# Performance work log

Measured on AMD Instinct MI355X. Metric: run time of the kernel, lower is better.

## Reference

```python
import jax, jax.numpy as jnp
import numpy as np

N, E, D_IN, D_H, N_CLASSES = 50000, 800000, 128, 128, 40
D_OUT = D_H // 2
LN_EPS = 1e-5


def _seg_mean(msgs, dst, n_nodes):
    # mean aggregation over incoming edges; isolated nodes get 0 (like PyG mean)
    s = jax.ops.segment_sum(msgs, dst, num_segments=n_nodes)
    cnt = jax.ops.segment_sum(jnp.ones((dst.shape[0], 1), msgs.dtype), dst, num_segments=n_nodes)
    return s / jnp.maximum(cnt, 1.0)


def _sage(x, src, dst, Wl, bl, Wr):
    # PyG SAGEConv(mean): lin_l(mean_j x_j) + lin_r(x_i); lin_l has bias, lin_r none
    agg = _seg_mean(x[src], dst, x.shape[0])  # [N, d_in]
    return agg @ Wl + bl + x @ Wr


def _layernorm(x, g, b):
    mu = jnp.mean(x, axis=-1, keepdims=True)
    var = jnp.mean(jnp.square(x - mu), axis=-1, keepdims=True)
    return (x - mu) * jax.lax.rsqrt(var + LN_EPS) * g + b


def setup_inputs() -> dict:
    key = jax.random.key(0)
    ks = jax.random.split(key, 20)
    sc = lambda d: 1.0 / np.sqrt(d)
    inp = {
        "x": jax.random.normal(ks[0], (N, D_IN), dtype=jnp.float32),
        "edge_index": jax.random.randint(ks[1], (2, E), 0, N, dtype=jnp.int32),
        # block1 (in==hidden -> proj is Identity)
        "Wl1": jax.random.normal(ks[2], (D_IN, D_H), jnp.float32) * sc(D_IN),
        "bl1": jnp.zeros((D_H,), jnp.float32),
        "Wr1": jax.random.normal(ks[3], (D_IN, D_H), jnp.float32) * sc(D_IN),
        "g1": jnp.ones((D_H,), jnp.float32),
        "b1": jnp.zeros((D_H,), jnp.float32),
        # block2
        "Wl2": jax.random.normal(ks[4], (D_H, D_H), jnp.float32) * sc(D_H),
        "bl2": jnp.zeros((D_H,), jnp.float32),
        "Wr2": jax.random.normal(ks[5], (D_H, D_H), jnp.float32) * sc(D_H),
        "g2": jnp.ones((D_H,), jnp.float32),
        "b2": jnp.zeros((D_H,), jnp.float32),
        # conv_out: hidden -> hidden//2
        "Wl3": jax.random.normal(ks[6], (D_H, D_OUT), jnp.float32) * sc(D_H),
        "bl3": jnp.zeros((D_OUT,), jnp.float32),
        "Wr3": jax.random.normal(ks[7], (D_H, D_OUT), jnp.float32) * sc(D_H),
        # classifier: LayerNorm(D_OUT) + Linear(D_OUT, n_classes)
        "gc": jnp.ones((D_OUT,), jnp.float32),
        "bc": jnp.zeros((D_OUT,), jnp.float32),
        "Wc": jax.random.normal(ks[8], (D_OUT, N_CLASSES), jnp.float32) * sc(D_OUT),
        "bcls": jnp.zeros((N_CLASSES,), jnp.float32),
    }
    return inp


def reference(x, edge_index, Wl1, bl1, Wr1, g1, b1, Wl2, bl2, Wr2, g2, b2,
              Wl3, bl3, Wr3, gc, bc, Wc, bcls):
    src, dst = edge_index[0], edge_index[1]
    # block1: SAGE -> LN -> GELU -> (dropout eval=identity) -> +x (proj=Identity)
    h = _sage(x, src, dst, Wl1, bl1, Wr1)
    x = jax.nn.gelu(_layernorm(h, g1, b1), approximate=False) + x
    # block2
    h = _sage(x, src, dst, Wl2, bl2, Wr2)
    x = jax.nn.gelu(_layernorm(h, g2, b2), approximate=False) + x
    # conv_out + GELU
    x = jax.nn.gelu(_sage(x, src, dst, Wl3, bl3, Wr3), approximate=False)
    # classifier: LN then Linear
    return _layernorm(x, gc, bc) @ Wc + bcls
```

## Files before the change

kernel.cpp:

```cpp
#include <hip/hip_runtime.h>
#include <math.h>


typedef __attribute__((ext_vector_type(8))) short bf16x8;
typedef __attribute__((ext_vector_type(4))) float f32x4;

#define NWG 256
#define NBK 196
#define CAP2 6144

__device__ inline float gelu_f(float x) {
    return 0.5f * x * (1.0f + erff(x * 0.70710678118654752440f));
}

__device__ inline ushort f2b(float f) {
    uint u = __float_as_uint(f);
    u += 0x7fffu + ((u >> 16) & 1u);
    return (ushort)(u >> 16);
}

__device__ inline float b2f(ushort h) { return __uint_as_float((uint)h << 16); }


__global__ __launch_bounds__(256) void k_hist(const int* __restrict__ dst, int e,
                                              int* __restrict__ cnts) {
    __shared__ int h[NBK];
    const int tid = threadIdx.x;
    const int wg = blockIdx.x;
    for (int i = tid; i < NBK; i += 256) h[i] = 0;
    __syncthreads();
    const int ch = (e + NWG - 1) / NWG;
    const int lo = wg * ch;
    const int hi = min(e, lo + ch);
    for (int i = lo + tid; i < hi; i += 256) atomicAdd(&h[dst[i] >> 8], 1);
    __syncthreads();
    for (int i = tid; i < NBK; i += 256) cnts[i * NWG + wg] = h[i];
}

__global__ __launch_bounds__(256) void k_scanP1(const int* __restrict__ in,
                                                int* __restrict__ out,
                                                int* __restrict__ part, int m) {
    __shared__ int sm[256];
    const int tid = threadIdx.x;
    const int base = blockIdx.x * 1024 + tid * 4;
    int4 v = make_int4(0, 0, 0, 0);
    if (base + 3 < m) {
        v = *(const int4*)(in + base);
    } else {
        if (base + 0 < m) v.x = in[base + 0];
        if (base + 1 < m) v.y = in[base + 1];
        if (base + 2 < m) v.z = in[base + 2];
        if (base + 3 < m) v.w = in[base + 3];
    }
    int s = v.x + v.y + v.z + v.w;
    sm[tid] = s;
    __syncthreads();
#pragma unroll
    for (int d = 1; d < 256; d <<= 1) {
        int add = (tid >= d) ? sm[tid - d] : 0;
        __syncthreads();
        sm[tid] += add;
        __syncthreads();
    }
    int ex = (tid ? sm[tid - 1] : 0);
    if (base + 0 < m) out[base + 0] = ex;
    ex += v.x;
    if (base + 1 < m) out[base + 1] = ex;
    ex += v.y;
    if (base + 2 < m) out[base + 2] = ex;
    ex += v.z;
    if (base + 3 < m) out[base + 3] = ex;
    if (tid == 255) part[blockIdx.x] = sm[255];
}

__global__ __launch_bounds__(256) void k_scanP2(int* __restrict__ out,
                                                const int* __restrict__ part, int m) {
    const int tid = threadIdx.x;
    const int bid = blockIdx.x;
    const int lane = tid & 63;
    int s = 0;
    for (int j = lane; j < bid; j += 64) s += part[j];
#pragma unroll
    for (int d = 32; d > 0; d >>= 1) s += __shfl_xor(s, d);
    const int i0 = bid * 1024 + tid * 4;
#pragma unroll
    for (int j = 0; j < 4; ++j) {
        int i = i0 + j;
        if (i < m) out[i] += s;
    }
}

__global__ __launch_bounds__(256) void k_scat(const int* __restrict__ src,
                                              const int* __restrict__ dst, int e,
                                              const int* __restrict__ bases,
                                              uint* __restrict__ pairs) {
    __shared__ int cur[NBK];
    const int tid = threadIdx.x;
    const int wg = blockIdx.x;
    for (int i = tid; i < NBK; i += 256) cur[i] = bases[i * NWG + wg];
    __syncthreads();
    const int ch = (e + NWG - 1) / NWG;
    const int lo = wg * ch;
    const int hi = min(e, lo + ch);
    for (int i = lo + tid; i < hi; i += 256) {
        int d = dst[i];
        int pos = atomicAdd(&cur[d >> 8], 1);
        pairs[pos] = (uint)src[i] | ((uint)(d & 255) << 16);
    }
}

__global__ __launch_bounds__(256) void k_sortC(const uint* __restrict__ pairs,
                                               const int* __restrict__ bases, int e,
                                               int* __restrict__ csr, int* __restrict__ off,
                                               int* __restrict__ cntout, int n) {
    __shared__ int hist[256];
    __shared__ int curl[256];
    __shared__ int sm[256];
    __shared__ int buf[CAP2];
    const int bk = blockIdx.x;
    const int tid = threadIdx.x;
    const int start = bases[bk * NWG];
    const int end = (bk == NBK - 1) ? e : bases[(bk + 1) * NWG];
    int m = end - start;
    if (m > CAP2) m = CAP2;

    hist[tid] = 0;
    __syncthreads();
    for (int i = tid; i < m; i += 256) atomicAdd(&hist[(pairs[start + i] >> 16) & 255], 1);
    __syncthreads();
    int v = hist[tid];
    sm[tid] = v;
    __syncthreads();
#pragma unroll
    for (int d = 1; d < 256; d <<= 1) {
        int add = (tid >= d) ? sm[tid - d] : 0;
        __syncthreads();
        sm[tid] += add;
        __syncthreads();
    }
    int excl = sm[tid] - v;
    int node = (bk << 8) + tid;
    if (node < n) {
        off[node] = start + excl;
        cntout[node] = v;
    }
    curl[tid] = excl;
    __syncthreads();
    for (int i = tid; i < m; i += 256) {
        uint w = pairs[start + i];
        int pos = atomicAdd(&curl[(w >> 16) & 255], 1);
        buf[pos] = (int)(w & 0xffffu);
    }
    __syncthreads();
    for (int i = tid; i < m; i += 256) csr[start + i] = buf[i];
}


__global__ void k_cast(const float* __restrict__ in, ushort* __restrict__ out, int nvec4) {
    int t = blockIdx.x * blockDim.x + threadIdx.x;
    int stride = gridDim.x * blockDim.x;
    for (int i = t; i < nvec4; i += stride) {
        float4 v = ((const float4*)in)[i];
        ushort4 o;
        o.x = f2b(v.x);
        o.y = f2b(v.y);
        o.z = f2b(v.z);
        o.w = f2b(v.w);
        ((ushort4*)out)[i] = o;
    }
}

__global__ void k_wprep(const float* __restrict__ Wl, const float* __restrict__ Wr,
                        int KH, int C, ushort* __restrict__ Wt) {
    int t = blockIdx.x * blockDim.x + threadIdx.x;
    int total = C * 2 * KH;
    if (t >= total) return;
    int c = t / (2 * KH), k = t % (2 * KH);
    float v = (k < KH) ? Wl[(size_t)k * C + c] : Wr[(size_t)(k - KH) * C + c];
    Wt[t] = f2b(v);
}

__global__ void k_wprepC(const float* __restrict__ Wc, ushort* __restrict__ Wct) {
    int t = blockIdx.x * blockDim.x + threadIdx.x;
    if (t >= 64 * 64) return;
    int c = t >> 6, k = t & 63;
    float v = (c < 40) ? Wc[k * 40 + c] : 0.f;
    Wct[t] = f2b(v);
}


__global__ void k_agg(const ushort* __restrict__ X, const int* __restrict__ off,
                      const int* __restrict__ cnt, const int* __restrict__ csr,
                      ushort* __restrict__ agg, int n) {
    const int wid = (blockIdx.x * blockDim.x + threadIdx.x) >> 6;
    const int lane = threadIdx.x & 63;
    const int nw = (gridDim.x * blockDim.x) >> 6;
    for (int i = wid; i < n; i += nw) {
        int s0 = off[i];
        int deg = cnt[i];
        int c = 0;
        if (lane < deg) c = csr[s0 + lane];
        float a0 = 0.f, a1 = 0.f;
        const int dcap = deg < 64 ? deg : 64;
        int t = 0;
        for (; t + 3 < dcap; t += 4) {
            int i0 = __shfl(c, t), i1 = __shfl(c, t + 1);
            int i2 = __shfl(c, t + 2), i3 = __shfl(c, t + 3);
            uint u0 = *((const uint*)(X + (size_t)i0 * 128) + lane);
            uint u1 = *((const uint*)(X + (size_t)i1 * 128) + lane);
            uint u2 = *((const uint*)(X + (size_t)i2 * 128) + lane);
            uint u3 = *((const uint*)(X + (size_t)i3 * 128) + lane);
            a0 += __uint_as_float(u0 << 16) + __uint_as_float(u1 << 16) +
                  __uint_as_float(u2 << 16) + __uint_as_float(u3 << 16);
            a1 += __uint_as_float(u0 & 0xffff0000u) + __uint_as_float(u1 & 0xffff0000u) +
                  __uint_as_float(u2 & 0xffff0000u) + __uint_as_float(u3 & 0xffff0000u);
        }
        for (; t < dcap; ++t) {
            uint u0 = *((const uint*)(X + (size_t)__shfl(c, t) * 128) + lane);
            a0 += __uint_as_float(u0 << 16);
            a1 += __uint_as_float(u0 & 0xffff0000u);
        }
        for (int tt = s0 + 64; tt < s0 + deg; ++tt) {
            uint u0 = *((const uint*)(X + (size_t)csr[tt] * 128) + lane);
            a0 += __uint_as_float(u0 << 16);
            a1 += __uint_as_float(u0 & 0xffff0000u);
        }
        float inv = 1.0f / (float)(deg > 1 ? deg : 1);
        uint pk = (uint)f2b(a0 * inv) | ((uint)f2b(a1 * inv) << 16);
        *((uint*)(agg + (size_t)i * 128) + lane) = pk;
    }
}


template <int DOUT, int EPI>
__global__ __launch_bounds__(256) void k_gemm(
    const ushort* __restrict__ Agg, const ushort* __restrict__ Xb,
    const ushort* __restrict__ Wt, const float* __restrict__ bias,
    const float* __restrict__ g, const float* __restrict__ b,
    ushort* __restrict__ OutB, int n) {
    constexpr int CT = DOUT / 64;
    const int tid = threadIdx.x;
    const int wave = tid >> 6;
    const int lane = tid & 63;
    const int l16 = lane & 15;
    const int g4 = lane >> 4;
    const int row0 = blockIdx.x * 32;

    __shared__ __align__(16) ushort As[32 * 256];

    int colv[CT];
#pragma unroll
    for (int ct = 0; ct < CT; ++ct) colv[ct] = (wave * CT + ct) * 16 + l16;

    bf16x8 bfr[CT][8];
#pragma unroll
    for (int ct = 0; ct < CT; ++ct) {
        const ushort* wp = Wt + (size_t)colv[ct] * 256 + g4 * 8;
#pragma unroll
        for (int ks = 0; ks < 8; ++ks) bfr[ct][ks] = *(const bf16x8*)(wp + ks * 32);
    }

    {
        const int row = tid >> 3;
        const int jj = tid & 7;
        int gr = row0 + row;
        if (gr > n - 1) gr = n - 1;
        const ushort* pa = Agg + (size_t)gr * 128;
        const ushort* pb = Xb + (size_t)gr * 128;
        uint4 v0 = *(const uint4*)(pa + jj * 8);
        uint4 v1 = *(const uint4*)(pa + (jj + 8) * 8);
        uint4 v2 = *(const uint4*)(pb + jj * 8);
        uint4 v3 = *(const uint4*)(pb + (jj + 8) * 8);
        const int sw = (row & 7) << 4;
        char* lb = (char*)As + row * 512;
        *(uint4*)(lb + ((jj * 16) ^ sw)) = v0;
        *(uint4*)(lb + (((jj + 8) * 16) ^ sw)) = v1;
        *(uint4*)(lb + (((jj + 16) * 16) ^ sw)) = v2;
        *(uint4*)(lb + (((jj + 24) * 16) ^ sw)) = v3;
    }

    float biasv[CT], gv[CT], bbv[CT];
#pragma unroll
    for (int ct = 0; ct < CT; ++ct) {
        biasv[ct] = bias[colv[ct]];
        gv[ct] = g[colv[ct]];
        bbv[ct] = b[colv[ct]];
    }

    __syncthreads();

    f32x4 acc[2][CT];
#pragma unroll
    for (int rt = 0; rt < 2; ++rt)
#pragma unroll
        for (int ct = 0; ct < CT; ++ct) {
            acc[rt][ct][0] = 0.f;
            acc[rt][ct][1] = 0.f;
            acc[rt][ct][2] = 0.f;
            acc[rt][ct][3] = 0.f;
        }
#pragma unroll
    for (int ks = 0; ks < 8; ++ks) {
        bf16x8 a[2];
#pragma unroll
        for (int rt = 0; rt < 2; ++rt) {
            const int row = rt * 16 + l16;
            a[rt] = *(const bf16x8*)((const char*)As + row * 512 +
                                     ((ks * 64 + g4 * 16) ^ ((row & 7) << 4)));
        }
#pragma unroll
        for (int rt = 0; rt < 2; ++rt)
#pragma unroll
            for (int ct = 0; ct < CT; ++ct)
                acc[rt][ct] = __builtin_amdgcn_mfma_f32_16x16x32_bf16(a[rt], bfr[ct][ks],
                                                                     acc[rt][ct], 0, 0, 0);
    }

    __shared__ float sP[32][4];
    __shared__ float qP[32][4];
    float v[2][4][CT];
    float sv[2][4], qv[2][4];
#pragma unroll
    for (int rt = 0; rt < 2; ++rt)
#pragma unroll
        for (int reg = 0; reg < 4; ++reg) {
            float s = 0.f, q = 0.f;
#pragma unroll
            for (int ct = 0; ct < CT; ++ct) {
                float t = acc[rt][ct][reg] + biasv[ct];
                if (EPI == 3) t = gelu_f(t);
                v[rt][reg][ct] = t;
                s += t;
                q += t * t;
            }
            sv[rt][reg] = s;
            qv[rt][reg] = q;
        }
#pragma unroll
    for (int m = 1; m < 16; m <<= 1)
#pragma unroll
        for (int rt = 0; rt < 2; ++rt)
#pragma unroll
            for (int reg = 0; reg < 4; ++reg) {
                sv[rt][reg] += __shfl_xor(sv[rt][reg], m);
                qv[rt][reg] += __shfl_xor(qv[rt][reg], m);
            }
    if (l16 == 0) {
#pragma unroll
        for (int rt = 0; rt < 2; ++rt)
#pragma unroll
            for (int reg = 0; reg < 4; ++reg) {
                int rib = rt * 16 + g4 * 4 + reg;
                sP[rib][wave] = sv[rt][reg];
                qP[rib][wave] = qv[rt][reg];
            }
    }
    __syncthreads();
#pragma unroll
    for (int rt = 0; rt < 2; ++rt) {
#pragma unroll
        for (int reg = 0; reg < 4; ++reg) {
            int rib = rt * 16 + g4 * 4 + reg;
            float s = sP[rib][0] + sP[rib][1] + sP[rib][2] + sP[rib][3];
            float q = qP[rib][0] + qP[rib][1] + qP[rib][2] + qP[rib][3];
            float mu = s * (1.0f / (float)DOUT);
            float var = q * (1.0f / (float)DOUT) - mu * mu;
            float rs = rsqrtf(fmaxf(var, 0.f) + 1e-5f);
            int r = row0 + rib;
            if (r >= n) continue;
#pragma unroll
            for (int ct = 0; ct < CT; ++ct) {
                float y = (v[rt][reg][ct] - mu) * rs * gv[ct] + bbv[ct];
                if (EPI == 1) {
                    ushort rh = *(const ushort*)((const char*)As + rib * 512 +
                                                 ((256 + 2 * colv[ct]) ^ ((rib & 7) << 4)));
                    y = gelu_f(y) + b2f(rh);
                }
                OutB[(size_t)r * DOUT + colv[ct]] = f2b(y);
            }
        }
    }
}


__global__ __launch_bounds__(256) void k_mm(const ushort* __restrict__ Y,
                                            const ushort* __restrict__ Wct,
                                            const float* __restrict__ bcls,
                                            float* __restrict__ Out, int n) {
    const int tid = threadIdx.x;
    const int wave = tid >> 6;
    const int lane = tid & 63;
    const int l16 = lane & 15;
    const int g4 = lane >> 4;
    const int row0 = blockIdx.x * 32;
    const int col = wave * 16 + l16;

    bf16x8 bfr[2];
#pragma unroll
    for (int ks = 0; ks < 2; ++ks)
        bfr[ks] = *(const bf16x8*)(Wct + (size_t)col * 64 + ks * 32 + g4 * 8);

    f32x4 acc[2];
#pragma unroll
    for (int rt = 0; rt < 2; ++rt) {
        acc[rt][0] = 0.f;
        acc[rt][1] = 0.f;
        acc[rt][2] = 0.f;
        acc[rt][3] = 0.f;
    }

    int arow[2];
#pragma unroll
    for (int rt = 0; rt < 2; ++rt) {
        int r = row0 + rt * 16 + l16;
        arow[rt] = (r < n) ? r : (n - 1);
    }

#pragma unroll
    for (int ks = 0; ks < 2; ++ks)
#pragma unroll
        for (int rt = 0; rt < 2; ++rt) {
            bf16x8 a = *(const bf16x8*)(Y + (size_t)arow[rt] * 64 + ks * 32 + g4 * 8);
            acc[rt] = __builtin_amdgcn_mfma_f32_16x16x32_bf16(a, bfr[ks], acc[rt], 0, 0, 0);
        }

    const float bcv = (col < 40) ? bcls[col] : 0.f;
#pragma unroll
    for (int rt = 0; rt < 2; ++rt)
#pragma unroll
        for (int reg = 0; reg < 4; ++reg) {
            int r = row0 + rt * 16 + g4 * 4 + reg;
            if (r < n && col < 40) Out[(size_t)r * 40 + col] = acc[rt][reg] + bcv;
        }
}


extern "C" void kernel_launch(void* const* d_in, const int* in_sizes, int n_in,
                              void* d_out, int out_size, void* d_ws, size_t ws_size,
                              hipStream_t stream) {
    const float* x   = (const float*)d_in[0];
    const int* ei    = (const int*)d_in[1];
    const float* Wl1 = (const float*)d_in[2];
    const float* bl1 = (const float*)d_in[3];
    const float* Wr1 = (const float*)d_in[4];
    const float* g1  = (const float*)d_in[5];
    const float* b1  = (const float*)d_in[6];
    const float* Wl2 = (const float*)d_in[7];
    const float* bl2 = (const float*)d_in[8];
    const float* Wr2 = (const float*)d_in[9];
    const float* g2  = (const float*)d_in[10];
    const float* b2  = (const float*)d_in[11];
    const float* Wl3 = (const float*)d_in[12];
    const float* bl3 = (const float*)d_in[13];
    const float* Wr3 = (const float*)d_in[14];
    const float* gc  = (const float*)d_in[15];
    const float* bc  = (const float*)d_in[16];
    const float* Wc  = (const float*)d_in[17];
    const float* bcls= (const float*)d_in[18];

    const int n = in_sizes[0] / 128;
    const int e = in_sizes[1] / 2;
    const int* src = ei;
    const int* dst = ei + e;

    char* w = (char*)d_ws;
    size_t o = 0;
    auto alloc = [&](size_t bytes) -> char* {
        char* p = w + o;
        o = (o + bytes + 511) & ~(size_t)511;
        return p;
    };
    int* cnts    = (int*)alloc((size_t)NBK * NWG * 4);
    int* bases   = (int*)alloc((size_t)NBK * NWG * 4);
    int* part    = (int*)alloc(256 * 4);
    uint* pairs  = (uint*)alloc((size_t)e * 4);
    int* csr     = (int*)alloc((size_t)e * 4);
    int* off     = (int*)alloc((size_t)n * 4);
    int* cnt     = (int*)alloc((size_t)n * 4);
    ushort* xB   = (ushort*)alloc((size_t)n * 128 * 2);
    ushort* aggB = (ushort*)alloc((size_t)n * 128 * 2);
    ushort* xaB  = (ushort*)alloc((size_t)n * 128 * 2);
    ushort* xbB  = (ushort*)alloc((size_t)n * 128 * 2);
    ushort* yB   = (ushort*)alloc((size_t)n * 64 * 2);
    ushort* W1t  = (ushort*)alloc((size_t)128 * 256 * 2);
    ushort* W2t  = (ushort*)alloc((size_t)128 * 256 * 2);
    ushort* W3t  = (ushort*)alloc((size_t)64 * 256 * 2);
    ushort* Wct  = (ushort*)alloc((size_t)64 * 64 * 2);
    (void)ws_size;

    const int m = NBK * NWG;
    const int sblk = (m + 1023) / 1024;
    k_hist<<<NWG, 256, 0, stream>>>(dst, e, cnts);
    k_scanP1<<<sblk, 256, 0, stream>>>(cnts, bases, part, m);
    k_scanP2<<<sblk, 256, 0, stream>>>(bases, part, m);
    k_scat<<<NWG, 256, 0, stream>>>(src, dst, e, bases, pairs);
    k_sortC<<<NBK, 256, 0, stream>>>(pairs, bases, e, csr, off, cnt, n);

    k_cast<<<2048, 256, 0, stream>>>(x, xB, n * 128 / 4);
    k_wprep<<<(128 * 256 + 255) / 256, 256, 0, stream>>>(Wl1, Wr1, 128, 128, W1t);
    k_wprep<<<(128 * 256 + 255) / 256, 256, 0, stream>>>(Wl2, Wr2, 128, 128, W2t);
    k_wprep<<<(64 * 256 + 255) / 256, 256, 0, stream>>>(Wl3, Wr3, 128, 64, W3t);
    k_wprepC<<<16, 256, 0, stream>>>(Wc, Wct);

    const int gg = (n + 31) / 32;

    k_agg<<<2048, 256, 0, stream>>>(xB, off, cnt, csr, aggB, n);
    k_gemm<128, 1><<<gg, 256, 0, stream>>>(aggB, xB, W1t, bl1, g1, b1, xaB, n);
    k_agg<<<2048, 256, 0, stream>>>(xaB, off, cnt, csr, aggB, n);
    k_gemm<128, 1><<<gg, 256, 0, stream>>>(aggB, xaB, W2t, bl2, g2, b2, xbB, n);
    k_agg<<<2048, 256, 0, stream>>>(xbB, off, cnt, csr, aggB, n);
    k_gemm<64, 3><<<gg, 256, 0, stream>>>(aggB, xbB, W3t, bl3, gc, bc, yB, n);
    k_mm<<<gg, 256, 0, stream>>>(yB, Wct, bcls, (float*)d_out, n);
}
```

Before: 204.5 us.

## Fuse neighbor mean aggregation into the SAGE GEMM kernel via shared memory

Removes the separate aggregation kernel and its global bf16 buffer. Each GEMM block now gathers and averages neighbor features for its 32 rows directly into the swizzled LDS tile (8 rows per wave), then runs the existing MFMA GEMM and epilogue. This saves the global write and re-read of the aggregate and one launch per layer. In exchange, the gather now runs with the GEMM's occupancy and grid (about 1563 blocks instead of a 2048-block grid-stride loop), so there is less latency hiding for the random gathers and the aggregation is serialized before the MMA inside each block.

```diff
diff --git a/kernel.cpp b/kernel.cpp
--- a/kernel.cpp
+++ b/kernel.cpp
@@ -189,52 +189,10 @@
 }
 
 
-__global__ void k_agg(const ushort* __restrict__ X, const int* __restrict__ off,
-                      const int* __restrict__ cnt, const int* __restrict__ csr,
-                      ushort* __restrict__ agg, int n) {
-    const int wid = (blockIdx.x * blockDim.x + threadIdx.x) >> 6;
-    const int lane = threadIdx.x & 63;
-    const int nw = (gridDim.x * blockDim.x) >> 6;
-    for (int i = wid; i < n; i += nw) {
-        int s0 = off[i];
-        int deg = cnt[i];
-        int c = 0;
-        if (lane < deg) c = csr[s0 + lane];
-        float a0 = 0.f, a1 = 0.f;
-        const int dcap = deg < 64 ? deg : 64;
-        int t = 0;
-        for (; t + 3 < dcap; t += 4) {
-            int i0 = __shfl(c, t), i1 = __shfl(c, t + 1);
-            int i2 = __shfl(c, t + 2), i3 = __shfl(c, t + 3);
-            uint u0 = *((const uint*)(X + (size_t)i0 * 128) + lane);
-            uint u1 = *((const uint*)(X + (size_t)i1 * 128) + lane);
-            uint u2 = *((const uint*)(X + (size_t)i2 * 128) + lane);
-            uint u3 = *((const uint*)(X + (size_t)i3 * 128) + lane);
-            a0 += __uint_as_float(u0 << 16) + __uint_as_float(u1 << 16) +
-                  __uint_as_float(u2 << 16) + __uint_as_float(u3 << 16);
-            a1 += __uint_as_float(u0 & 0xffff0000u) + __uint_as_float(u1 & 0xffff0000u) +
-                  __uint_as_float(u2 & 0xffff0000u) + __uint_as_float(u3 & 0xffff0000u);
-        }
-        for (; t < dcap; ++t) {
-            uint u0 = *((const uint*)(X + (size_t)__shfl(c, t) * 128) + lane);
-            a0 += __uint_as_float(u0 << 16);
-            a1 += __uint_as_float(u0 & 0xffff0000u);
-        }
-        for (int tt = s0 + 64; tt < s0 + deg; ++tt) {
-            uint u0 = *((const uint*)(X + (size_t)csr[tt] * 128) + lane);
-            a0 += __uint_as_float(u0 << 16);
-            a1 += __uint_as_float(u0 & 0xffff0000u);
-        }
-        float inv = 1.0f / (float)(deg > 1 ? deg : 1);
-        uint pk = (uint)f2b(a0 * inv) | ((uint)f2b(a1 * inv) << 16);
-        *((uint*)(agg + (size_t)i * 128) + lane) = pk;
-    }
-}
-
-
 template <int DOUT, int EPI>
-__global__ __launch_bounds__(256) void k_gemm(
-    const ushort* __restrict__ Agg, const ushort* __restrict__ Xb,
+__global__ __launch_bounds__(256) void k_fused(
+    const ushort* __restrict__ X, const int* __restrict__ off,
+    const int* __restrict__ cnt, const int* __restrict__ csr,
     const ushort* __restrict__ Wt, const float* __restrict__ bias,
     const float* __restrict__ g, const float* __restrict__ b,
     ushort* __restrict__ OutB, int n) {
@@ -265,18 +223,55 @@
         const int jj = tid & 7;
         int gr = row0 + row;
         if (gr > n - 1) gr = n - 1;
-        const ushort* pa = Agg + (size_t)gr * 128;
-        const ushort* pb = Xb + (size_t)gr * 128;
-        uint4 v0 = *(const uint4*)(pa + jj * 8);
-        uint4 v1 = *(const uint4*)(pa + (jj + 8) * 8);
+        const ushort* pb = X + (size_t)gr * 128;
         uint4 v2 = *(const uint4*)(pb + jj * 8);
         uint4 v3 = *(const uint4*)(pb + (jj + 8) * 8);
         const int sw = (row & 7) << 4;
         char* lb = (char*)As + row * 512;
-        *(uint4*)(lb + ((jj * 16) ^ sw)) = v0;
-        *(uint4*)(lb + (((jj + 8) * 16) ^ sw)) = v1;
         *(uint4*)(lb + (((jj + 16) * 16) ^ sw)) = v2;
         *(uint4*)(lb + (((jj + 24) * 16) ^ sw)) = v3;
+    }
+
+#pragma unroll 1
+    for (int j = 0; j < 8; ++j) {
+        const int ri = wave * 8 + j;
+        const int i = row0 + ri;
+        uint pk = 0;
+        if (i < n) {
+            int s0 = off[i];
+            int deg = cnt[i];
+            int c = 0;
+            if (lane < deg) c = csr[s0 + lane];
+            float a0 = 0.f, a1 = 0.f;
+            const int dcap = deg < 64 ? deg : 64;
+            int t = 0;
+            for (; t + 3 < dcap; t += 4) {
+                int i0 = __shfl(c, t), i1 = __shfl(c, t + 1);
+                int i2 = __shfl(c, t + 2), i3 = __shfl(c, t + 3);
+                uint u0 = *((const uint*)(X + (size_t)i0 * 128) + lane);
+                uint u1 = *((const uint*)(X + (size_t)i1 * 128) + lane);
+                uint u2 = *((const uint*)(X + (size_t)i2 * 128) + lane);
+                uint u3 = *((const uint*)(X + (size_t)i3 * 128) + lane);
+                a0 += __uint_as_float(u0 << 16) + __uint_as_float(u1 << 16) +
+                      __uint_as_float(u2 << 16) + __uint_as_float(u3 << 16);
+                a1 += __uint_as_float(u0 & 0xffff0000u) + __uint_as_float(u1 & 0xffff0000u) +
+                      __uint_as_float(u2 & 0xffff0000u) + __uint_as_float(u3 & 0xffff0000u);
+            }
+            for (; t < dcap; ++t) {
+                uint u0 = *((const uint*)(X + (size_t)__shfl(c, t) * 128) + lane);
+                a0 += __uint_as_float(u0 << 16);
+                a1 += __uint_as_float(u0 & 0xffff0000u);
+            }
+            for (int tt = s0 + 64; tt < s0 + deg; ++tt) {
+                uint u0 = *((const uint*)(X + (size_t)csr[tt] * 128) + lane);
+                a0 += __uint_as_float(u0 << 16);
+                a1 += __uint_as_float(u0 & 0xffff0000u);
+            }
+            float inv = 1.0f / (float)(deg > 1 ? deg : 1);
+            pk = (uint)f2b(a0 * inv) | ((uint)f2b(a1 * inv) << 16);
+        }
+        char* lbr = (char*)As + ri * 512;
+        *(uint*)(lbr + ((lane * 4) ^ ((ri & 7) << 4))) = pk;
     }
 
     float biasv[CT], gv[CT], bbv[CT];
@@ -478,7 +473,6 @@
     int* off     = (int*)alloc((size_t)n * 4);
     int* cnt     = (int*)alloc((size_t)n * 4);
     ushort* xB   = (ushort*)alloc((size_t)n * 128 * 2);
-    ushort* aggB = (ushort*)alloc((size_t)n * 128 * 2);
     ushort* xaB  = (ushort*)alloc((size_t)n * 128 * 2);
     ushort* xbB  = (ushort*)alloc((size_t)n * 128 * 2);
     ushort* yB   = (ushort*)alloc((size_t)n * 64 * 2);
@@ -504,11 +498,8 @@
 
     const int gg = (n + 31) / 32;
 
-    k_agg<<<2048, 256, 0, stream>>>(xB, off, cnt, csr, aggB, n);
-    k_gemm<128, 1><<<gg, 256, 0, stream>>>(aggB, xB, W1t, bl1, g1, b1, xaB, n);
-    k_agg<<<2048, 256, 0, stream>>>(xaB, off, cnt, csr, aggB, n);
-    k_gemm<128, 1><<<gg, 256, 0, stream>>>(aggB, xaB, W2t, bl2, g2, b2, xbB, n);
-    k_agg<<<2048, 256, 0, stream>>>(xbB, off, cnt, csr, aggB, n);
-    k_gemm<64, 3><<<gg, 256, 0, stream>>>(aggB, xbB, W3t, bl3, gc, bc, yB, n);
+    k_fused<128, 1><<<gg, 256, 0, stream>>>(xB, off, cnt, csr, W1t, bl1, g1, b1, xaB, n);
+    k_fused<128, 1><<<gg, 256, 0, stream>>>(xaB, off, cnt, csr, W2t, bl2, g2, b2, xbB, n);
+    k_fused<64, 3><<<gg, 256, 0, stream>>>(xbB, off, cnt, csr, W3t, bl3, gc, bc, yB, n);
     k_mm<<<gg, 256, 0, stream>>>(yB, Wct, bcls, (float*)d_out, n);
 }
```

Result: slower. 261.2 us (+27.7%).
